# Kernel optimization log

Hardware: AMD Instinct MI355X
Metric: run time of the kernel (lower is better)

## Reference

```python
import jax, jax.numpy as jnp
import numpy as np


def setup_inputs() -> dict:
    key = jax.random.key(0)
    kq, kk, kv = jax.random.split(key, 3)
    shape = (2, 8, 1024, 64)  # [B, H, L, D]
    return {
        "q": jax.random.normal(kq, shape, dtype=jnp.float32),
        "k": jax.random.normal(kk, shape, dtype=jnp.float32),
        "v": jax.random.normal(kv, shape, dtype=jnp.float32),
    }


def reference(q, k, v):
    B, H, L, D = q.shape
    eps = 1e-6
    q = jax.nn.relu(q).reshape(B * H, L, D)
    k = jax.nn.relu(k).reshape(B * H, L, D)
    v = jax.nn.relu(v).reshape(B * H, L, D)

    # cosFormer positional reweighting: pi/2 * (i+1)/L
    idx = (jnp.pi / 2) * jnp.arange(1, L + 1, dtype=q.dtype) / L  # [L]
    s = jnp.sin(idx)[None, :, None]  # [1, L, 1]
    c = jnp.cos(idx)[None, :, None]

    q_ = jnp.concatenate([q * s, q * c], axis=-1)  # [N, L, 2D]
    k_ = jnp.concatenate([k * s, k * c], axis=-1)  # [N, L, 2D]

    # causal linear attention via cumulative kv outer product
    kv = jnp.einsum("nld,nlm->nldm", k_, v)        # [N, L, 2D, D]
    kv_cum = jnp.cumsum(kv, axis=1)                  # [N, L, 2D, D]
    qkv = jnp.einsum("nld,nldm->nlm", q_, kv_cum)  # [N, L, D]

    k_cum = jnp.cumsum(k_, axis=1)                   # [N, L, 2D]
    denom = jnp.clip(jnp.einsum("nld,nld->nl", q_, k_cum), eps, None)

    out = qkv / denom[..., None]
    return out.reshape(B, H, L, D)
```

## Files before the change

kernel.cpp:

```cpp
#include <hip/hip_runtime.h>
#include <hip/hip_fp16.h>

#define N_HEADS 16
#define L_SEQ   1024
#define D_HEAD  64
#define D2      128
#define T_CHUNK 32
#define N_CHUNK (L_SEQ / T_CHUNK)
#define KV_ELEMS (D2 * D_HEAD)
#define PK_UINTS (KV_ELEMS / 2)

#define ROWP 140
__device__ __forceinline__ int pad_col(int d2) { return d2 + 4 * (d2 >> 5); }

#define PQ 132
#define PS 136
#define PV 36

#define SINCOS_SCALE 1.53398078788564122971e-3f

typedef _Float16 f16_t;
typedef __attribute__((ext_vector_type(4))) _Float16 f16x4;
typedef __attribute__((ext_vector_type(4))) float f32x4;

__device__ __forceinline__ f32x4 mfma16(f16x4 a, f16x4 b, f32x4 c) {
    return __builtin_amdgcn_mfma_f32_16x16x16f16(a, b, c, 0, 0, 0);
}

__device__ __forceinline__ unsigned int packh2(float a, float b) {
    __half2 h = __floats2half2_rn(a, b);
    return __builtin_bit_cast(unsigned int, h);
}
__device__ __forceinline__ float2 unpackh2(unsigned int u) {
    __half2 h = __builtin_bit_cast(__half2, u);
    return __half22float2(h);
}

__device__ __forceinline__ float red8_dpp(float x) {
    x += __int_as_float(__builtin_amdgcn_mov_dpp(__float_as_int(x), 0xB1, 0xF, 0xF, true));
    x += __int_as_float(__builtin_amdgcn_mov_dpp(__float_as_int(x), 0x4E, 0xF, 0xF, true));
    x += __int_as_float(__builtin_amdgcn_mov_dpp(__float_as_int(x), 0x141, 0xF, 0xF, true));
    return x;
}
__device__ __forceinline__ float red16_dpp(float x) {
    x += __int_as_float(__builtin_amdgcn_mov_dpp(__float_as_int(x), 0xB1, 0xF, 0xF, true));
    x += __int_as_float(__builtin_amdgcn_mov_dpp(__float_as_int(x), 0x4E, 0xF, 0xF, true));
    x += __int_as_float(__builtin_amdgcn_mov_dpp(__float_as_int(x), 0x141, 0xF, 0xF, true));
    x += __int_as_float(__builtin_amdgcn_mov_dpp(__float_as_int(x), 0x140, 0xF, 0xF, true));
    return x;
}

__global__ __launch_bounds__(256, 2) void k1_chunk_sums(
    const float* __restrict__ k, const float* __restrict__ v,
    unsigned int* __restrict__ sumkv, float* __restrict__ sumk)
{
    __shared__ __attribute__((aligned(16))) float k_s[T_CHUNK][ROWP];
    __shared__ __attribute__((aligned(16))) float v_s[T_CHUNK][D_HEAD];
    __shared__ float s_tab[T_CHUNK], c_tab[T_CHUNK];

    const int c = blockIdx.x, n = blockIdx.y;
    const int tid = threadIdx.x;
    const int base = (n * L_SEQ + c * T_CHUNK) * D_HEAD;

    if (tid < T_CHUNK) {
        float th = SINCOS_SCALE * (float)(c * T_CHUNK + tid + 1);
        s_tab[tid] = __sinf(th);
        c_tab[tid] = __cosf(th);
    }
    __syncthreads();

    const float4* k4g = (const float4*)(k + base);
    const float4* v4g = (const float4*)(v + base);
#pragma unroll
    for (int j = 0; j < 2; ++j) {
        int i4 = j * 256 + tid;
        int l = i4 >> 4, d = (i4 & 15) << 2;
        float4 kk = k4g[i4], vv = v4g[i4];
        kk.x = fmaxf(kk.x, 0.f); kk.y = fmaxf(kk.y, 0.f);
        kk.z = fmaxf(kk.z, 0.f); kk.w = fmaxf(kk.w, 0.f);
        vv.x = fmaxf(vv.x, 0.f); vv.y = fmaxf(vv.y, 0.f);
        vv.z = fmaxf(vv.z, 0.f); vv.w = fmaxf(vv.w, 0.f);
        float s = s_tab[l], cs = c_tab[l];
        *(float4*)&k_s[l][pad_col(d)]      = make_float4(kk.x*s,  kk.y*s,  kk.z*s,  kk.w*s);
        *(float4*)&k_s[l][pad_col(d + 64)] = make_float4(kk.x*cs, kk.y*cs, kk.z*cs, kk.w*cs);
        *(float4*)&v_s[l][d] = vv;
    }
    __syncthreads();

    if (tid < D2) {
        int pc = pad_col(tid);
        float ks = 0.f;
#pragma unroll
        for (int l = 0; l < T_CHUNK; ++l) ks += k_s[l][pc];
        sumk[(n * N_CHUNK + c) * D2 + tid] = ks;
    }

    const int g = tid & 7, mh = (tid >> 3) << 1;
    const int gbase = pad_col(16 * g);

    float st0[16], st1[16];
#pragma unroll
    for (int j = 0; j < 16; ++j) { st0[j] = 0.f; st1[j] = 0.f; }

    for (int l = 0; l < T_CHUNK; ++l) {
        float2 vm = *(const float2*)&v_s[l][mh];
        const float4* kv4 = (const float4*)&k_s[l][gbase];
#pragma unroll
        for (int jj = 0; jj < 4; ++jj) {
            float4 kk = kv4[jj];
            st0[4*jj+0] = fmaf(kk.x, vm.x, st0[4*jj+0]);
            st1[4*jj+0] = fmaf(kk.x, vm.y, st1[4*jj+0]);
            st0[4*jj+1] = fmaf(kk.y, vm.x, st0[4*jj+1]);
            st1[4*jj+1] = fmaf(kk.y, vm.y, st1[4*jj+1]);
            st0[4*jj+2] = fmaf(kk.z, vm.x, st0[4*jj+2]);
            st1[4*jj+2] = fmaf(kk.z, vm.y, st1[4*jj+2]);
            st0[4*jj+3] = fmaf(kk.w, vm.x, st0[4*jj+3]);
            st1[4*jj+3] = fmaf(kk.w, vm.y, st1[4*jj+3]);
        }
    }

    uint4* dst = (uint4*)(sumkv + (size_t)(n * N_CHUNK + c) * PK_UINTS);
    {
        int i0 = mh * 16 + (g << 1);
        int i1 = i0 + 16;
        dst[i0]     = make_uint4(packh2(st0[0],st0[1]),   packh2(st0[2],st0[3]),
                                 packh2(st0[4],st0[5]),   packh2(st0[6],st0[7]));
        dst[i0 + 1] = make_uint4(packh2(st0[8],st0[9]),   packh2(st0[10],st0[11]),
                                 packh2(st0[12],st0[13]), packh2(st0[14],st0[15]));
        dst[i1]     = make_uint4(packh2(st1[0],st1[1]),   packh2(st1[2],st1[3]),
                                 packh2(st1[4],st1[5]),   packh2(st1[6],st1[7]));
        dst[i1 + 1] = make_uint4(packh2(st1[8],st1[9]),   packh2(st1[10],st1[11]),
                                 packh2(st1[12],st1[13]), packh2(st1[14],st1[15]));
    }
}

__global__ __launch_bounds__(256) void k2_prefix(
    unsigned int* __restrict__ sumkv, float* __restrict__ sumk)
{
    const int x = blockIdx.x, n = blockIdx.y;
    const int tid = threadIdx.x;

    if (x < 8) {
        uint2* base = (uint2*)(sumkv + (size_t)n * N_CHUNK * PK_UINTS) + x * 256 + tid;
        uint2 t[N_CHUNK];
#pragma unroll
        for (int c = 0; c < N_CHUNK; ++c) t[c] = base[c * (PK_UINTS / 2)];
        float r0 = 0.f, r1 = 0.f, r2 = 0.f, r3 = 0.f;
#pragma unroll
        for (int c = 0; c < N_CHUNK; ++c) {
            uint2 cur = t[c];
            base[c * (PK_UINTS / 2)] = make_uint2(packh2(r0, r1), packh2(r2, r3));
            float2 lo = unpackh2(cur.x), hi = unpackh2(cur.y);
            r0 += lo.x; r1 += lo.y; r2 += hi.x; r3 += hi.y;
        }
    } else if (tid < D2) {
        float* bk = sumk + n * N_CHUNK * D2 + tid;
        float t[N_CHUNK];
#pragma unroll
        for (int c = 0; c < N_CHUNK; ++c) t[c] = bk[c * D2];
        float r = 0.f;
#pragma unroll
        for (int c = 0; c < N_CHUNK; ++c) { bk[c * D2] = r; r += t[c]; }
    }
}

__global__ __launch_bounds__(256, 2) void k3_output(
    const float* __restrict__ q, const float* __restrict__ k,
    const float* __restrict__ v, const unsigned int* __restrict__ sumkv,
    const float* __restrict__ sumk, float* __restrict__ out)
{
    __shared__ __attribute__((aligned(16))) f16_t q16[T_CHUNK][PQ];
    __shared__ __attribute__((aligned(16))) f16_t k16[T_CHUNK][PQ];
    __shared__ __attribute__((aligned(16))) f16_t vt[D_HEAD][PV];
    __shared__ __attribute__((aligned(16))) f16_t s0t[D_HEAD][PS];
    __shared__ __attribute__((aligned(16))) f16_t pmat[T_CHUNK][PV];
    __shared__ float kc0[D2];
    __shared__ float den0_s[T_CHUNK], dpA[T_CHUNK], dpB[T_CHUNK], rden[T_CHUNK];
    __shared__ float s_tab[T_CHUNK], c_tab[T_CHUNK];

    const int c = blockIdx.x, n = blockIdx.y;
    const int tid = threadIdx.x;
    const int base = (n * L_SEQ + c * T_CHUNK) * D_HEAD;

    if (tid < T_CHUNK) {
        float th = SINCOS_SCALE * (float)(c * T_CHUNK + tid + 1);
        s_tab[tid] = __sinf(th);
        c_tab[tid] = __cosf(th);
    }
    __syncthreads();

    const float4* q4g = (const float4*)(q + base);
    const float4* k4g = (const float4*)(k + base);
    const float4* v4g = (const float4*)(v + base);
#pragma unroll
    for (int j = 0; j < 2; ++j) {
        int i4 = j * 256 + tid;
        int l = i4 >> 4, d = (i4 & 15) << 2;
        float4 kk = k4g[i4], qq = q4g[i4], vv = v4g[i4];
        kk.x = fmaxf(kk.x, 0.f); kk.y = fmaxf(kk.y, 0.f);
        kk.z = fmaxf(kk.z, 0.f); kk.w = fmaxf(kk.w, 0.f);
        qq.x = fmaxf(qq.x, 0.f); qq.y = fmaxf(qq.y, 0.f);
        qq.z = fmaxf(qq.z, 0.f); qq.w = fmaxf(qq.w, 0.f);
        vv.x = fmaxf(vv.x, 0.f); vv.y = fmaxf(vv.y, 0.f);
        vv.z = fmaxf(vv.z, 0.f); vv.w = fmaxf(vv.w, 0.f);
        float s = s_tab[l], cs = c_tab[l];
        q16[l][d+0]    = (f16_t)(qq.x*s);  q16[l][d+1]    = (f16_t)(qq.y*s);
        q16[l][d+2]    = (f16_t)(qq.z*s);  q16[l][d+3]    = (f16_t)(qq.w*s);
        q16[l][d+64]   = (f16_t)(qq.x*cs); q16[l][d+65]   = (f16_t)(qq.y*cs);
        q16[l][d+66]   = (f16_t)(qq.z*cs); q16[l][d+67]   = (f16_t)(qq.w*cs);
        k16[l][d+0]    = (f16_t)(kk.x*s);  k16[l][d+1]    = (f16_t)(kk.y*s);
        k16[l][d+2]    = (f16_t)(kk.z*s);  k16[l][d+3]    = (f16_t)(kk.w*s);
        k16[l][d+64]   = (f16_t)(kk.x*cs); k16[l][d+65]   = (f16_t)(kk.y*cs);
        k16[l][d+66]   = (f16_t)(kk.z*cs); k16[l][d+67]   = (f16_t)(kk.w*cs);
        vt[d+0][l] = (f16_t)vv.x; vt[d+1][l] = (f16_t)vv.y;
        vt[d+2][l] = (f16_t)vv.z; vt[d+3][l] = (f16_t)vv.w;
    }
    {
        const uint4* pkv = (const uint4*)(sumkv + (size_t)(n * N_CHUNK + c) * PK_UINTS);
#pragma unroll
        for (int jj = 0; jj < 4; ++jj) {
            int u = jj * 256 + tid;
            int pos = u << 3;
            *(uint4*)&s0t[pos >> 7][pos & 127] = pkv[u];
        }
    }
    if (tid < D2) kc0[tid] = sumk[(n * N_CHUNK + c) * D2 + tid];
    __syncthreads();

    {
        int l = tid >> 3, seg = (tid & 7) << 4;
        float a = 0.f;
#pragma unroll
        for (int i = 0; i < 16; ++i) a += (float)q16[l][seg + i] * kc0[seg + i];
        a = red8_dpp(a);
        if ((tid & 7) == 0) den0_s[l] = a;
    }

    const int wave = tid >> 6, lane = tid & 63;
    const int fr = lane & 15;
    const int fk = (lane >> 4) << 2;
    const int rowq = (lane >> 4) << 2;

    if (wave < 3) {
        const int mt = (wave == 0) ? 0 : 1;
        const int nt = (wave == 2) ? 1 : 0;
        f32x4 sa = {0.f, 0.f, 0.f, 0.f};
#pragma unroll
        for (int ks = 0; ks < 8; ++ks) {
            f16x4 a = *(const f16x4*)&q16[mt * 16 + fr][ks * 16 + fk];
            f16x4 b = *(const f16x4*)&k16[nt * 16 + fr][ks * 16 + fk];
            sa = mfma16(a, b, sa);
        }
#pragma unroll
        for (int r = 0; r < 4; ++r) {
            int row = rowq + r;
            float mv = (mt > nt || fr <= row) ? sa[r] : 0.f;
            pmat[mt * 16 + row][nt * 16 + fr] = (f16_t)mv;
            float rs = red16_dpp(mv);
            if (fr == 0) {
                if (wave == 2) dpB[16 + row] = rs;
                else dpA[mt * 16 + row] = rs;
            }
        }
    } else {
        int row = lane >> 2, colb = 16 + ((lane & 3) << 2);
        *(uint2*)&pmat[row][colb] = make_uint2(0u, 0u);
    }
    __syncthreads();

    if (tid < T_CHUNK) {
        float den = den0_s[tid] + dpA[tid] + ((tid >= 16) ? dpB[tid] : 0.f);
        rden[tid] = 1.f / fmaxf(den, 1e-6f);
    }

    const int mt = wave >> 1;
    const int nt0 = (wave & 1) << 1, nt1 = nt0 + 1;
    f32x4 o0 = {0.f, 0.f, 0.f, 0.f}, o1 = {0.f, 0.f, 0.f, 0.f};
#pragma unroll
    for (int ks = 0; ks < 8; ++ks) {
        f16x4 a  = *(const f16x4*)&q16[mt * 16 + fr][ks * 16 + fk];
        f16x4 b0 = *(const f16x4*)&s0t[nt0 * 16 + fr][ks * 16 + fk];
        f16x4 b1 = *(const f16x4*)&s0t[nt1 * 16 + fr][ks * 16 + fk];
        o0 = mfma16(a, b0, o0);
        o1 = mfma16(a, b1, o1);
    }
#pragma unroll
    for (int ks = 0; ks < 2; ++ks) {
        f16x4 a  = *(const f16x4*)&pmat[mt * 16 + fr][ks * 16 + fk];
        f16x4 b0 = *(const f16x4*)&vt[nt0 * 16 + fr][ks * 16 + fk];
        f16x4 b1 = *(const f16x4*)&vt[nt1 * 16 + fr][ks * 16 + fk];
        o0 = mfma16(a, b0, o0);
        o1 = mfma16(a, b1, o1);
    }
    __syncthreads();

    float* og = out + base;
#pragma unroll
    for (int r = 0; r < 4; ++r) {
        int row = mt * 16 + rowq + r;
        float rd = rden[row];
        og[row * D_HEAD + nt0 * 16 + fr] = o0[r] * rd;
        og[row * D_HEAD + nt1 * 16 + fr] = o1[r] * rd;
    }
}

extern "C" void kernel_launch(void* const* d_in, const int* in_sizes, int n_in,
                              void* d_out, int out_size, void* d_ws, size_t ws_size,
                              hipStream_t stream) {
    (void)in_sizes; (void)n_in; (void)out_size; (void)ws_size;
    const float* q = (const float*)d_in[0];
    const float* k = (const float*)d_in[1];
    const float* v = (const float*)d_in[2];
    float* out = (float*)d_out;

    unsigned int* sumkv = (unsigned int*)d_ws;
    float* sumk = (float*)(sumkv + (size_t)N_HEADS * N_CHUNK * PK_UINTS);

    dim3 grid(N_CHUNK, N_HEADS);
    k1_chunk_sums<<<grid, 256, 0, stream>>>(k, v, sumkv, sumk);
    dim3 grid2(9, N_HEADS);
    k2_prefix<<<grid2, 256, 0, stream>>>(sumkv, sumk);
    k3_output<<<grid, 256, 0, stream>>>(q, k, v, sumkv, sumk, out);
}
```

Baseline: 79.03 us.

## Compute per-chunk KV outer-product sums with fp16 MFMA instead of scalar FMA

```diff
diff --git a/kernel.cpp b/kernel.cpp
--- a/kernel.cpp
+++ b/kernel.cpp
@@ -10,9 +10,6 @@
 #define KV_ELEMS (D2 * D_HEAD)
 #define PK_UINTS (KV_ELEMS / 2)
 
-#define ROWP 140
-__device__ __forceinline__ int pad_col(int d2) { return d2 + 4 * (d2 >> 5); }
-
 #define PQ 132
 #define PS 136
 #define PV 36
@@ -54,8 +51,9 @@
     const float* __restrict__ k, const float* __restrict__ v,
     unsigned int* __restrict__ sumkv, float* __restrict__ sumk)
 {
-    __shared__ __attribute__((aligned(16))) float k_s[T_CHUNK][ROWP];
-    __shared__ __attribute__((aligned(16))) float v_s[T_CHUNK][D_HEAD];
+    __shared__ __attribute__((aligned(16))) f16_t k16t[D2][PV];
+    __shared__ __attribute__((aligned(16))) f16_t vt1[D_HEAD][PV];
+    __shared__ __attribute__((aligned(16))) f16_t ob[D_HEAD][PS];
     __shared__ float s_tab[T_CHUNK], c_tab[T_CHUNK];
 
     const int c = blockIdx.x, n = blockIdx.y;
@@ -81,56 +79,56 @@
         vv.x = fmaxf(vv.x, 0.f); vv.y = fmaxf(vv.y, 0.f);
         vv.z = fmaxf(vv.z, 0.f); vv.w = fmaxf(vv.w, 0.f);
         float s = s_tab[l], cs = c_tab[l];
-        *(float4*)&k_s[l][pad_col(d)]      = make_float4(kk.x*s,  kk.y*s,  kk.z*s,  kk.w*s);
-        *(float4*)&k_s[l][pad_col(d + 64)] = make_float4(kk.x*cs, kk.y*cs, kk.z*cs, kk.w*cs);
-        *(float4*)&v_s[l][d] = vv;
+        k16t[d+0][l]    = (f16_t)(kk.x*s);  k16t[d+1][l]    = (f16_t)(kk.y*s);
+        k16t[d+2][l]    = (f16_t)(kk.z*s);  k16t[d+3][l]    = (f16_t)(kk.w*s);
+        k16t[d+64][l]   = (f16_t)(kk.x*cs); k16t[d+65][l]   = (f16_t)(kk.y*cs);
+        k16t[d+66][l]   = (f16_t)(kk.z*cs); k16t[d+67][l]   = (f16_t)(kk.w*cs);
+        vt1[d+0][l] = (f16_t)vv.x; vt1[d+1][l] = (f16_t)vv.y;
+        vt1[d+2][l] = (f16_t)vv.z; vt1[d+3][l] = (f16_t)vv.w;
     }
     __syncthreads();
 
     if (tid < D2) {
-        int pc = pad_col(tid);
-        float ks = 0.f;
-#pragma unroll
-        for (int l = 0; l < T_CHUNK; ++l) ks += k_s[l][pc];
-        sumk[(n * N_CHUNK + c) * D2 + tid] = ks;
-    }
-
-    const int g = tid & 7, mh = (tid >> 3) << 1;
-    const int gbase = pad_col(16 * g);
-
-    float st0[16], st1[16];
-#pragma unroll
-    for (int j = 0; j < 16; ++j) { st0[j] = 0.f; st1[j] = 0.f; }
-
-    for (int l = 0; l < T_CHUNK; ++l) {
-        float2 vm = *(const float2*)&v_s[l][mh];
-        const float4* kv4 = (const float4*)&k_s[l][gbase];
-#pragma unroll
-        for (int jj = 0; jj < 4; ++jj) {
-            float4 kk = kv4[jj];
-            st0[4*jj+0] = fmaf(kk.x, vm.x, st0[4*jj+0]);
-            st1[4*jj+0] = fmaf(kk.x, vm.y, st1[4*jj+0]);
-            st0[4*jj+1] = fmaf(kk.y, vm.x, st0[4*jj+1]);
-            st1[4*jj+1] = fmaf(kk.y, vm.y, st1[4*jj+1]);
-            st0[4*jj+2] = fmaf(kk.z, vm.x, st0[4*jj+2]);
-            st1[4*jj+2] = fmaf(kk.z, vm.y, st1[4*jj+2]);
-            st0[4*jj+3] = fmaf(kk.w, vm.x, st0[4*jj+3]);
-            st1[4*jj+3] = fmaf(kk.w, vm.y, st1[4*jj+3]);
-        }
-    }
+        const f16x4* row = (const f16x4*)&k16t[tid][0];
+        float acc = 0.f;
+#pragma unroll
+        for (int i = 0; i < 8; ++i) {
+            f16x4 x = row[i];
+            acc += ((float)x[0] + (float)x[1]) + ((float)x[2] + (float)x[3]);
+        }
+        sumk[(n * N_CHUNK + c) * D2 + tid] = acc;
+    }
+
+    const int wave = tid >> 6, lane = tid & 63;
+    const int fr = lane & 15;
+    const int fk = (lane >> 4) << 2;
+
+    f16x4 a0 = *(const f16x4*)&vt1[wave * 16 + fr][fk];
+    f16x4 a1 = *(const f16x4*)&vt1[wave * 16 + fr][16 + fk];
+
+    f32x4 acc[8];
+#pragma unroll
+    for (int nt = 0; nt < 8; ++nt) acc[nt] = (f32x4){0.f, 0.f, 0.f, 0.f};
+#pragma unroll
+    for (int nt = 0; nt < 8; ++nt) {
+        f16x4 b0 = *(const f16x4*)&k16t[nt * 16 + fr][fk];
+        f16x4 b1 = *(const f16x4*)&k16t[nt * 16 + fr][16 + fk];
+        acc[nt] = mfma16(a0, b0, acc[nt]);
+        acc[nt] = mfma16(a1, b1, acc[nt]);
+    }
+
+#pragma unroll
+    for (int nt = 0; nt < 8; ++nt)
+#pragma unroll
+        for (int r = 0; r < 4; ++r)
+            ob[wave * 16 + fk + r][nt * 16 + fr] = (f16_t)acc[nt][r];
+    __syncthreads();
 
     uint4* dst = (uint4*)(sumkv + (size_t)(n * N_CHUNK + c) * PK_UINTS);
-    {
-        int i0 = mh * 16 + (g << 1);
-        int i1 = i0 + 16;
-        dst[i0]     = make_uint4(packh2(st0[0],st0[1]),   packh2(st0[2],st0[3]),
-                                 packh2(st0[4],st0[5]),   packh2(st0[6],st0[7]));
-        dst[i0 + 1] = make_uint4(packh2(st0[8],st0[9]),   packh2(st0[10],st0[11]),
-                                 packh2(st0[12],st0[13]), packh2(st0[14],st0[15]));
-        dst[i1]     = make_uint4(packh2(st1[0],st1[1]),   packh2(st1[2],st1[3]),
-                                 packh2(st1[4],st1[5]),   packh2(st1[6],st1[7]));
-        dst[i1 + 1] = make_uint4(packh2(st1[8],st1[9]),   packh2(st1[10],st1[11]),
-                                 packh2(st1[12],st1[13]), packh2(st1[14],st1[15]));
+#pragma unroll
+    for (int t = 0; t < 4; ++t) {
+        int u = t * 256 + tid;
+        dst[u] = *(const uint4*)&ob[u >> 4][(u & 15) * 8];
     }
 }
 
```

New measurement: 75.59 us (median of 2 runs). -4.4%, faster.
